# Optimization experiments

Measured on AMD Instinct MI355X. Metric: run time of the kernel, lower is better.

Reference implementation:

```python
import jax, jax.numpy as jnp
import numpy as np
import math

D_MODEL = 1024
N_HEADS = 16
D_HEAD = D_MODEL // N_HEADS
B, T = 2, 2048


def setup_inputs() -> dict:
    key = jax.random.key(0)
    ks = jax.random.split(key, 5)
    x = jax.random.normal(ks[0], (B, T, D_MODEL), dtype=jnp.float32)
    W_qkv = jax.random.normal(ks[1], (D_MODEL, 3 * D_MODEL), dtype=jnp.float32) * 0.02
    b_qkv = jnp.zeros((3 * D_MODEL,), dtype=jnp.float32)
    W_g = jax.random.normal(ks[2], (N_HEADS, D_HEAD, D_HEAD), dtype=jnp.float32) * 0.02
    W_out = jax.random.normal(ks[3], (D_MODEL, D_MODEL), dtype=jnp.float32) * 0.02
    b_out = jnp.zeros((D_MODEL,), dtype=jnp.float32)
    return {"x": x, "W_qkv": W_qkv, "b_qkv": b_qkv, "W_g": W_g, "W_out": W_out, "b_out": b_out}


def reference(x, W_qkv, b_qkv, W_g, W_out, b_out):
    b, t, d = x.shape
    h, dh = N_HEADS, D_HEAD
    qkv = x @ W_qkv + b_qkv                         # (B,T,3D)
    q, k, v = jnp.split(qkv, 3, axis=-1)
    # (B,T,D) -> (B,H,T,dh)
    q = q.reshape(b, t, h, dh).transpose(0, 2, 1, 3)
    k = k.reshape(b, t, h, dh).transpose(0, 2, 1, 3)
    v = v.reshape(b, t, h, dh).transpose(0, 2, 1, 3)
    scale = 1.0 / math.sqrt(dh)
    scores = jnp.einsum('bhtd,bhsd->bhts', q, k) * scale   # (B,H,T,T)
    causal = jnp.tril(jnp.ones((t, t), dtype=bool))
    scores = jnp.where(causal, scores, jnp.float32(-jnp.inf))
    attn = jax.nn.softmax(scores, axis=-1)
    # query-conditioned bilinear value gate (applied at each position)
    g = jax.nn.sigmoid(jnp.einsum('bhtd,hde->bhte', q, W_g))  # (B,H,T,dh)
    v = g * v
    out = jnp.einsum('bhts,bhsd->bhtd', attn, v)             # (B,H,T,dh)
    out = out.transpose(0, 2, 1, 3).reshape(b, t, d)
    return out @ W_out + b_out
```

## Files before the change

kernel.cpp:

```cpp
#include <hip/hip_runtime.h>
#include <hip/hip_bf16.h>

typedef unsigned short ushortT;
typedef __bf16 bf16x8 __attribute__((ext_vector_type(8)));
typedef __bf16 bf16x4 __attribute__((ext_vector_type(4)));
typedef float f32x4 __attribute__((ext_vector_type(4)));

#define T_SEQ 2048
#define DH 64
#define NH 16
#define DM 1024
#define TD 3072
#define BATCH 2
#define LOG2E 1.44269504f

__device__ inline ushortT f2bf(float f){
    union { float f; unsigned int u; } a; a.f = f;
    unsigned int r = a.u + 0x7fffu + ((a.u >> 16) & 1u);
    return (ushortT)(r >> 16);
}
__device__ inline float bf2f(ushortT u){
    union { float f; unsigned int u; } a; a.u = ((unsigned int)u) << 16;
    return a.f;
}

__device__ inline void gload_lds16(const void* g, void* l){
    __builtin_amdgcn_global_load_lds((const __attribute__((address_space(1))) void*)g,
                                     (__attribute__((address_space(3))) void*)l, 16, 0, 0);
}

__global__ __launch_bounds__(256) void cast_bf16_kernel(const float* __restrict__ in,
                                                        ushortT* __restrict__ out, int n){
    int i = (blockIdx.x * 256 + threadIdx.x) * 4;
    if (i < n){
        float4 v = *(const float4*)&in[i];
        out[i+0] = f2bf(v.x); out[i+1] = f2bf(v.y);
        out[i+2] = f2bf(v.z); out[i+3] = f2bf(v.w);
    }
}

__global__ __launch_bounds__(256) void transcast_kernel(const float* __restrict__ in,
                                                        ushortT* __restrict__ out, int K, int N){
    __shared__ float tile[64][65];
    int n0 = blockIdx.x * 64, k0 = blockIdx.y * 64;
    int tid = threadIdx.x;
    int c  = tid & 63;
    int r4 = tid >> 6;
#pragma unroll
    for (int i = 0; i < 16; i++){
        int k = r4 + i * 4;
        tile[k][c] = in[(size_t)(k0 + k) * N + n0 + c];
    }
    __syncthreads();
#pragma unroll
    for (int i = 0; i < 16; i++){
        int n = r4 + i * 4;
        out[(size_t)(n0 + n) * K + k0 + c] = f2bf(tile[c][n]);
    }
}

__global__ __launch_bounds__(256) void wg_transcast_kernel(const float* __restrict__ in,
                                                           ushortT* __restrict__ out){
    __shared__ float tile[64][65];
    int h = blockIdx.x;
    int tid = threadIdx.x;
    int c = tid & 63, r4 = tid >> 6;
#pragma unroll
    for (int i = 0; i < 16; i++){
        int d = r4 + i*4;
        tile[d][c] = in[h*4096 + d*64 + c];
    }
    __syncthreads();
#pragma unroll
    for (int i = 0; i < 16; i++){
        int e = r4 + i*4;
        out[h*4096 + e*64 + c] = f2bf(tile[c][e]);
    }
}

__device__ inline void store_out(ushortT* C, size_t i, float v){ C[i] = f2bf(v); }
__device__ inline void store_out(float*   C, size_t i, float v){ C[i] = v; }

template <typename OUT>
__global__ __launch_bounds__(256) void gemm_bf16_kernel(const ushortT* __restrict__ A,
                                                        const ushortT* __restrict__ BT,
                                                        const float* __restrict__ bias,
                                                        OUT* __restrict__ C,
                                                        int M, int N, int K){
    __shared__ __align__(16) ushortT As[2][128*32];
    __shared__ __align__(16) ushortT Bs[2][128*32];
    int tid = threadIdx.x;
    int m0 = blockIdx.x * 128;
    int n0 = blockIdx.y * 128;
    int wid = tid >> 6, lane = tid & 63;
    int l15 = lane & 15, g = lane >> 4;
    int wr = wid >> 1, wc = wid & 1;

    f32x4 acc[4][4];
#pragma unroll
    for (int i = 0; i < 4; i++)
#pragma unroll
        for (int j = 0; j < 4; j++) acc[i][j] = (f32x4){0.f,0.f,0.f,0.f};

    int srow = wid * 32 + (lane >> 2);
    int sch  = lane & 3;

#define GSTAGE(buf, k0)                                                                  \
    {                                                                                    \
        _Pragma("unroll")                                                                \
        for (int i_ = 0; i_ < 2; i_++){                                                  \
            int row_ = srow + i_ * 16;                                                   \
            const ushortT* asrc_ = A  + (size_t)(m0 + row_) * K + (k0) + sch * 8;        \
            const ushortT* bsrc_ = BT + (size_t)(n0 + row_) * K + (k0) + sch * 8;        \
            gload_lds16(asrc_, (char*)As[buf] + (wid*2 + i_) * 1024);                    \
            gload_lds16(bsrc_, (char*)Bs[buf] + (wid*2 + i_) * 1024);                    \
        }                                                                                \
    }

    GSTAGE(0, 0);
    __syncthreads();

    int nk = K >> 5;
    for (int kt = 0; kt < nk; kt++){
        int buf = kt & 1;
        if (kt + 1 < nk) GSTAGE(buf ^ 1, (kt + 1) * 32);

        bf16x8 af[4], bfr[4];
#pragma unroll
        for (int mi = 0; mi < 4; mi++){
            int r = wr*64 + mi*16 + l15;
            af[mi]  = *(const bf16x8*)(As[buf] + r*32 + g*8);
        }
#pragma unroll
        for (int ni = 0; ni < 4; ni++){
            int r = wc*64 + ni*16 + l15;
            bfr[ni] = *(const bf16x8*)(Bs[buf] + r*32 + g*8);
        }
#pragma unroll
        for (int mi = 0; mi < 4; mi++)
#pragma unroll
            for (int ni = 0; ni < 4; ni++)
                acc[mi][ni] = __builtin_amdgcn_mfma_f32_16x16x32_bf16(af[mi], bfr[ni], acc[mi][ni], 0, 0, 0);
        __syncthreads();
    }
#undef GSTAGE

#pragma unroll
    for (int mi = 0; mi < 4; mi++){
#pragma unroll
        for (int jj = 0; jj < 4; jj++){
            int mm = m0 + wr*64 + mi*16 + 4*g + jj;
#pragma unroll
            for (int ni = 0; ni < 4; ni++){
                int nn = n0 + wc*64 + ni*16 + l15;
                float v = acc[mi][ni][jj] + bias[nn];
                store_out(C, (size_t)mm * N + nn, v);
            }
        }
    }
}

__global__ __launch_bounds__(256) void gate_kernel(const ushortT* __restrict__ qkv,
                                                   const ushortT* __restrict__ WgT,
                                                   ushortT* __restrict__ vgT){
    __shared__ __align__(16) ushortT VT[64][72];
    int tblk = blockIdx.x, bh = blockIdx.y;
    int b = bh >> 4, h = bh & 15;
    int tid = threadIdx.x, wid = tid >> 6, lane = tid & 63;
    int l15 = lane & 15, g = lane >> 4;
    int t0 = tblk * 64;
    int tl = wid*16 + l15;

    const ushortT* qrow = qkv + ((size_t)b*T_SEQ + t0 + tl)*TD + h*DH;
    bf16x8 qf0 = *(const bf16x8*)(qrow + 8*g);
    bf16x8 qf1 = *(const bf16x8*)(qrow + 32 + 8*g);

    const ushortT* wbase = WgT + h*4096;
    const ushortT* vrow = qkv + ((size_t)b*T_SEQ + t0 + tl)*TD + 2*DM + h*DH;

#pragma unroll
    for (int ns = 0; ns < 4; ns++){
        int e = ns*16 + l15;
        bf16x8 wf0 = *(const bf16x8*)(wbase + e*64 + 8*g);
        bf16x8 wf1 = *(const bf16x8*)(wbase + e*64 + 32 + 8*g);
        f32x4 z = (f32x4){0.f,0.f,0.f,0.f};
        z = __builtin_amdgcn_mfma_f32_16x16x32_bf16(wf0, qf0, z, 0, 0, 0);
        z = __builtin_amdgcn_mfma_f32_16x16x32_bf16(wf1, qf1, z, 0, 0, 0);
        union { ushortT u[4]; uint2 v; } v4;
        v4.v = *(const uint2*)(vrow + ns*16 + 4*g);
#pragma unroll
        for (int jj = 0; jj < 4; jj++){
            float ex = __builtin_amdgcn_exp2f(-z[jj] * LOG2E);
            float gv = __builtin_amdgcn_rcpf(1.f + ex);
            VT[ns*16 + 4*g + jj][tl] = f2bf(gv * bf2f(v4.u[jj]));
        }
    }
    __syncthreads();
    for (int i = tid; i < 64*8; i += 256){
        int e = i >> 3, c8 = (i & 7) * 8;
        *(uint4*)&vgT[((size_t)bh * DH + e) * T_SEQ + t0 + c8] = *(const uint4*)&VT[e][c8];
    }
}

struct QState {
    bf16x8 qf0, qf1;
    float m_, lsum;
    f32x4 acc[4];
};

__device__ __forceinline__ void proc_tile(const ushortT* __restrict__ Kb,
                                          const ushortT* __restrict__ Vb,
                                          QState& S, bool diag,
                                          int wg, int l15, int g,
                                          ushortT (*Pl)[72], float* Al){
    f32x4 s[4];
    __builtin_amdgcn_s_setprio(1);
#pragma unroll
    for (int ns = 0; ns < 4; ns++){
        int kr = ns*16 + l15;
        bf16x8 kf0 = *(const bf16x8*)(Kb + kr*64 + ((g     ) ^ (kr & 7))*8);
        bf16x8 kf1 = *(const bf16x8*)(Kb + kr*64 + ((4 + g) ^ (kr & 7))*8);
        f32x4 z = (f32x4){0.f,0.f,0.f,0.f};
        z = __builtin_amdgcn_mfma_f32_16x16x32_bf16(kf0, S.qf0, z, 0, 0, 0);
        z = __builtin_amdgcn_mfma_f32_16x16x32_bf16(kf1, S.qf1, z, 0, 0, 0);
        s[ns] = z;
    }
    __builtin_amdgcn_s_setprio(0);

    float tmax = -INFINITY;
    if (diag){
        int qrel = wg*16 + l15;
#pragma unroll
        for (int ns = 0; ns < 4; ns++){
            int kbase = ns*16 + 4*g;
#pragma unroll
            for (int jj = 0; jj < 4; jj++){
                if (kbase + jj > qrel) s[ns][jj] = -INFINITY;
                tmax = fmaxf(tmax, s[ns][jj]);
            }
        }
    } else {
#pragma unroll
        for (int ns = 0; ns < 4; ns++){
            float a = fmaxf(s[ns][0], s[ns][1]);
            float c = fmaxf(s[ns][2], s[ns][3]);
            tmax = fmaxf(tmax, fmaxf(a, c));
        }
    }
    tmax = fmaxf(tmax, __shfl_xor(tmax, 16, 64));
    tmax = fmaxf(tmax, __shfl_xor(tmax, 32, 64));

    float mnew = fmaxf(S.m_, tmax);
    float mc = mnew * LOG2E;
    float rs = 0.f;
#pragma unroll
    for (int ns = 0; ns < 4; ns++){
        bf16x4 pk;
#pragma unroll
        for (int jj = 0; jj < 4; jj++){
            float p = __builtin_amdgcn_exp2f(fmaf(s[ns][jj], LOG2E, -mc));
            pk[jj] = (__bf16)p;
            rs += p;
        }
        *(bf16x4*)&Pl[l15][ns*16 + 4*g] = pk;
    }
    rs += __shfl_xor(rs, 16, 64);
    rs += __shfl_xor(rs, 32, 64);

    if (!__all(mnew == S.m_)){
        float alpha = __builtin_amdgcn_exp2f(fmaf(S.m_, LOG2E, -mc));
        Al[l15] = alpha;
        f32x4 a4 = *(const f32x4*)&Al[4*g];
#pragma unroll
        for (int nt = 0; nt < 4; nt++)
#pragma unroll
            for (int jj = 0; jj < 4; jj++) S.acc[nt][jj] *= a4[jj];
        S.lsum *= alpha;
        S.m_ = mnew;
    }
    S.lsum += rs;

    __builtin_amdgcn_s_setprio(1);
#pragma unroll
    for (int ks = 0; ks < 2; ks++){
        bf16x8 pa = *(const bf16x8*)&Pl[l15][ks*32 + 8*g];
#pragma unroll
        for (int nt = 0; nt < 4; nt++){
            int e = nt*16 + l15;
            bf16x8 vf = *(const bf16x8*)(Vb + e*64 + ((ks*4 + g) ^ (e & 7))*8);
            S.acc[nt] = __builtin_amdgcn_mfma_f32_16x16x32_bf16(pa, vf, S.acc[nt], 0, 0, 0);
        }
    }
    __builtin_amdgcn_s_setprio(0);
}

__global__ __launch_bounds__(512) void attn_kernel(const ushortT* __restrict__ qkv,
                                                   const ushortT* __restrict__ vgT,
                                                   ushortT* __restrict__ obf){
    __shared__ __align__(16) ushortT Ks[2][64*64];
    __shared__ __align__(16) ushortT Vs[2][64*64];
    __shared__ __align__(16) ushortT Plds[8][16][72];
    __shared__ __align__(16) float Alds[8][16];
    int bh = blockIdx.x, pairid = blockIdx.y;
    int b = bh >> 4, h = bh & 15;
    int tid = threadIdx.x, wid = tid >> 6, lane = tid & 63;
    int l15 = lane & 15, g = lane >> 4;
    int grp = wid >> 2, wg = wid & 3;

    const ushortT* Kg = qkv + (size_t)b * T_SEQ * TD + DM + h * DH;
    const ushortT* Vg = vgT + (size_t)bh * DH * T_SEQ;

    int st_row = wid*8 + (lane >> 3);
    int st_c   = (lane & 7) ^ ((lane >> 3) & 7);

#define STAGE_TILE(bufidx, kv0)                                                          \
    {                                                                                    \
        const ushortT* ksrc_ = Kg + (size_t)((kv0) + st_row) * TD + st_c*8;              \
        const ushortT* vsrc_ = Vg + (size_t)st_row * T_SEQ + (kv0) + st_c*8;             \
        gload_lds16(ksrc_, (char*)Ks[bufidx] + wid*1024);                                \
        gload_lds16(vsrc_, (char*)Vs[bufidx] + wid*1024);                                \
    }

    int pA = pairid, pB = 31 - pairid;
    int myp = grp ? pB : pA;

    QState S;
    {
        int qrow = myp*64 + wg*16 + l15;
        const ushortT* qb = qkv + ((size_t)b * T_SEQ + qrow) * TD + h * DH;
        S.qf0 = *(const bf16x8*)(qb + 8*g);
        S.qf1 = *(const bf16x8*)(qb + 32 + 8*g);
    }
#pragma unroll
    for (int j = 0; j < 8; j++){
        S.qf0[j] = (__bf16)((float)S.qf0[j] * 0.125f);
        S.qf1[j] = (__bf16)((float)S.qf1[j] * 0.125f);
    }
    S.m_ = -INFINITY; S.lsum = 0.f;
#pragma unroll
    for (int nt = 0; nt < 4; nt++) S.acc[nt] = (f32x4){0.f,0.f,0.f,0.f};

    STAGE_TILE(0, 0);
    __syncthreads();

    for (int t = 0; t <= pB; t++){
        int buf = t & 1;
        if (t < pB) STAGE_TILE(buf ^ 1, (t+1)*64);
        if (t <= myp)
            proc_tile(Ks[buf], Vs[buf], S, t == myp, wg, l15, g, Plds[wid], Alds[wid]);
        __syncthreads();
    }
#undef STAGE_TILE

    Alds[wid][l15] = 1.f / S.lsum;
    f32x4 i4 = *(const f32x4*)&Alds[wid][4*g];
#pragma unroll
    for (int jj = 0; jj < 4; jj++){
        int t = myp*64 + wg*16 + 4*g + jj;
#pragma unroll
        for (int nt = 0; nt < 4; nt++)
            obf[((size_t)b * T_SEQ + t) * DM + h*DH + nt*16 + l15] =
                f2bf(S.acc[nt][jj] * i4[jj]);
    }
}

extern "C" void kernel_launch(void* const* d_in, const int* in_sizes, int n_in,
                              void* d_out, int out_size, void* d_ws, size_t ws_size,
                              hipStream_t stream){
    const float* x    = (const float*)d_in[0];
    const float* Wqkv = (const float*)d_in[1];
    const float* bqkv = (const float*)d_in[2];
    const float* Wg   = (const float*)d_in[3];
    const float* Wout = (const float*)d_in[4];
    const float* bout = (const float*)d_in[5];

    char* ws = (char*)d_ws;
    ushortT* xbf   = (ushortT*)(ws);
    ushortT* wqkvT = (ushortT*)(ws + 8388608);
    ushortT* woutT = (ushortT*)(ws + 14680064);
    ushortT* qkvb  = (ushortT*)(ws + 16777216);
    ushortT* vgT   = (ushortT*)(ws + 41943040);
    ushortT* obf   = (ushortT*)(ws + 50331648);
    ushortT* wgT   = (ushortT*)(ws + 58720256);

    cast_bf16_kernel<<<4096, 256, 0, stream>>>(x, xbf, 4194304);
    transcast_kernel<<<dim3(48,16), 256, 0, stream>>>(Wqkv, wqkvT, 1024, 3072);
    transcast_kernel<<<dim3(16,16), 256, 0, stream>>>(Wout, woutT, 1024, 1024);
    wg_transcast_kernel<<<16, 256, 0, stream>>>(Wg, wgT);
    gemm_bf16_kernel<ushortT><<<dim3(32,24), 256, 0, stream>>>(xbf, wqkvT, bqkv, qkvb, 4096, 3072, 1024);
    gate_kernel<<<dim3(32,32), 256, 0, stream>>>(qkvb, wgT, vgT);
    attn_kernel<<<dim3(32,16), 512, 0, stream>>>(qkvb, vgT, obf);
    gemm_bf16_kernel<float><<<dim3(32,8), 256, 0, stream>>>(obf, woutT, bout, (float*)d_out, 4096, 1024, 1024);
}
```

Measured before the change: 126.4 us.

## Keep softmax probabilities in registers by permuting K rows and swapping MFMA operands

Staging now loads K rows in a permuted order, and the PV MFMA takes its operands swapped, so the exp'd score fragments already match the A-operand layout. The probabilities stay in registers instead of going through an LDS round trip, and the per-row alpha/inverse-sum broadcasts through LDS also go away. The output is written as packed 8-byte stores, and the grid is flattened to 1D with a remapped block-to-(bh,pair) order that may change scheduling balance and L2 locality. The permuted indexing and causal-mask offsets must agree exactly or the results will be wrong.

```diff
diff --git a/kernel.cpp b/kernel.cpp
--- a/kernel.cpp
+++ b/kernel.cpp
@@ -211,15 +211,15 @@
 __device__ __forceinline__ void proc_tile(const ushortT* __restrict__ Kb,
                                           const ushortT* __restrict__ Vb,
                                           QState& S, bool diag,
-                                          int wg, int l15, int g,
-                                          ushortT (*Pl)[72], float* Al){
+                                          int wg, int l15, int g){
+    int l7 = l15 & 7;
     f32x4 s[4];
     __builtin_amdgcn_s_setprio(1);
 #pragma unroll
     for (int ns = 0; ns < 4; ns++){
         int kr = ns*16 + l15;
-        bf16x8 kf0 = *(const bf16x8*)(Kb + kr*64 + ((g     ) ^ (kr & 7))*8);
-        bf16x8 kf1 = *(const bf16x8*)(Kb + kr*64 + ((4 + g) ^ (kr & 7))*8);
+        bf16x8 kf0 = *(const bf16x8*)(Kb + kr*64 + ((g    ) ^ l7)*8);
+        bf16x8 kf1 = *(const bf16x8*)(Kb + kr*64 + ((4 + g) ^ l7)*8);
         f32x4 z = (f32x4){0.f,0.f,0.f,0.f};
         z = __builtin_amdgcn_mfma_f32_16x16x32_bf16(kf0, S.qf0, z, 0, 0, 0);
         z = __builtin_amdgcn_mfma_f32_16x16x32_bf16(kf1, S.qf1, z, 0, 0, 0);
@@ -232,7 +232,7 @@
         int qrel = wg*16 + l15;
 #pragma unroll
         for (int ns = 0; ns < 4; ns++){
-            int kbase = ns*16 + 4*g;
+            int kbase = ((ns & 2) << 4) + 8*g + ((ns & 1) << 2);
 #pragma unroll
             for (int jj = 0; jj < 4; jj++){
                 if (kbase + jj > qrel) s[ns][jj] = -INFINITY;
@@ -253,28 +253,28 @@
     float mnew = fmaxf(S.m_, tmax);
     float mc = mnew * LOG2E;
     float rs = 0.f;
-#pragma unroll
-    for (int ns = 0; ns < 4; ns++){
-        bf16x4 pk;
-#pragma unroll
-        for (int jj = 0; jj < 4; jj++){
-            float p = __builtin_amdgcn_exp2f(fmaf(s[ns][jj], LOG2E, -mc));
-            pk[jj] = (__bf16)p;
-            rs += p;
-        }
-        *(bf16x4*)&Pl[l15][ns*16 + 4*g] = pk;
+    bf16x8 pa0, pa1;
+#pragma unroll
+    for (int jj = 0; jj < 4; jj++){
+        float p0 = __builtin_amdgcn_exp2f(fmaf(s[0][jj], LOG2E, -mc));
+        float p1 = __builtin_amdgcn_exp2f(fmaf(s[1][jj], LOG2E, -mc));
+        float p2 = __builtin_amdgcn_exp2f(fmaf(s[2][jj], LOG2E, -mc));
+        float p3 = __builtin_amdgcn_exp2f(fmaf(s[3][jj], LOG2E, -mc));
+        rs += (p0 + p1) + (p2 + p3);
+        pa0[jj]   = (__bf16)p0;
+        pa0[4+jj] = (__bf16)p1;
+        pa1[jj]   = (__bf16)p2;
+        pa1[4+jj] = (__bf16)p3;
     }
     rs += __shfl_xor(rs, 16, 64);
     rs += __shfl_xor(rs, 32, 64);
 
     if (!__all(mnew == S.m_)){
         float alpha = __builtin_amdgcn_exp2f(fmaf(S.m_, LOG2E, -mc));
-        Al[l15] = alpha;
-        f32x4 a4 = *(const f32x4*)&Al[4*g];
 #pragma unroll
         for (int nt = 0; nt < 4; nt++)
 #pragma unroll
-            for (int jj = 0; jj < 4; jj++) S.acc[nt][jj] *= a4[jj];
+            for (int jj = 0; jj < 4; jj++) S.acc[nt][jj] *= alpha;
         S.lsum *= alpha;
         S.m_ = mnew;
     }
@@ -283,12 +283,11 @@
     __builtin_amdgcn_s_setprio(1);
 #pragma unroll
     for (int ks = 0; ks < 2; ks++){
-        bf16x8 pa = *(const bf16x8*)&Pl[l15][ks*32 + 8*g];
+        bf16x8 pa = ks ? pa1 : pa0;
 #pragma unroll
         for (int nt = 0; nt < 4; nt++){
-            int e = nt*16 + l15;
-            bf16x8 vf = *(const bf16x8*)(Vb + e*64 + ((ks*4 + g) ^ (e & 7))*8);
-            S.acc[nt] = __builtin_amdgcn_mfma_f32_16x16x32_bf16(pa, vf, S.acc[nt], 0, 0, 0);
+            bf16x8 vf = *(const bf16x8*)(Vb + (nt*16 + l15)*64 + ((ks*4 + g) ^ l7)*8);
+            S.acc[nt] = __builtin_amdgcn_mfma_f32_16x16x32_bf16(vf, pa, S.acc[nt], 0, 0, 0);
         }
     }
     __builtin_amdgcn_s_setprio(0);
@@ -299,9 +298,11 @@
                                                    ushortT* __restrict__ obf){
     __shared__ __align__(16) ushortT Ks[2][64*64];
     __shared__ __align__(16) ushortT Vs[2][64*64];
-    __shared__ __align__(16) ushortT Plds[8][16][72];
-    __shared__ __align__(16) float Alds[8][16];
-    int bh = blockIdx.x, pairid = blockIdx.y;
+    int id = blockIdx.x;
+    int half = id >> 8, j = id & 255;
+    int bh = (half << 4) | (j >> 4);
+    int pp = j & 15;
+    int pairid = half ? (15 - pp) : pp;
     int b = bh >> 4, h = bh & 15;
     int tid = threadIdx.x, wid = tid >> 6, lane = tid & 63;
     int l15 = lane & 15, g = lane >> 4;
@@ -312,10 +313,11 @@
 
     int st_row = wid*8 + (lane >> 3);
     int st_c   = (lane & 7) ^ ((lane >> 3) & 7);
+    int st_prow = (st_row & 0x20) | ((st_row & 0x0C) << 1) | ((st_row & 0x10) >> 2) | (st_row & 3);
 
 #define STAGE_TILE(bufidx, kv0)                                                          \
     {                                                                                    \
-        const ushortT* ksrc_ = Kg + (size_t)((kv0) + st_row) * TD + st_c*8;              \
+        const ushortT* ksrc_ = Kg + (size_t)((kv0) + st_prow) * TD + st_c*8;             \
         const ushortT* vsrc_ = Vg + (size_t)st_row * T_SEQ + (kv0) + st_c*8;             \
         gload_lds16(ksrc_, (char*)Ks[bufidx] + wid*1024);                                \
         gload_lds16(vsrc_, (char*)Vs[bufidx] + wid*1024);                                \
@@ -332,9 +334,9 @@
         S.qf1 = *(const bf16x8*)(qb + 32 + 8*g);
     }
 #pragma unroll
-    for (int j = 0; j < 8; j++){
-        S.qf0[j] = (__bf16)((float)S.qf0[j] * 0.125f);
-        S.qf1[j] = (__bf16)((float)S.qf1[j] * 0.125f);
+    for (int jq = 0; jq < 8; jq++){
+        S.qf0[jq] = (__bf16)((float)S.qf0[jq] * 0.125f);
+        S.qf1[jq] = (__bf16)((float)S.qf1[jq] * 0.125f);
     }
     S.m_ = -INFINITY; S.lsum = 0.f;
 #pragma unroll
@@ -347,20 +349,19 @@
         int buf = t & 1;
         if (t < pB) STAGE_TILE(buf ^ 1, (t+1)*64);
         if (t <= myp)
-            proc_tile(Ks[buf], Vs[buf], S, t == myp, wg, l15, g, Plds[wid], Alds[wid]);
+            proc_tile(Ks[buf], Vs[buf], S, t == myp, wg, l15, g);
         __syncthreads();
     }
 #undef STAGE_TILE
 
-    Alds[wid][l15] = 1.f / S.lsum;
-    f32x4 i4 = *(const f32x4*)&Alds[wid][4*g];
-#pragma unroll
-    for (int jj = 0; jj < 4; jj++){
-        int t = myp*64 + wg*16 + 4*g + jj;
-#pragma unroll
-        for (int nt = 0; nt < 4; nt++)
-            obf[((size_t)b * T_SEQ + t) * DM + h*DH + nt*16 + l15] =
-                f2bf(S.acc[nt][jj] * i4[jj]);
+    float inv = 1.f / S.lsum;
+    size_t orow = ((size_t)b * T_SEQ + myp*64 + wg*16 + l15) * DM + h*DH;
+#pragma unroll
+    for (int nt = 0; nt < 4; nt++){
+        union { ushortT u[4]; uint2 v; } pk;
+#pragma unroll
+        for (int jj = 0; jj < 4; jj++) pk.u[jj] = f2bf(S.acc[nt][jj] * inv);
+        *(uint2*)&obf[orow + nt*16 + 4*g] = pk.v;
     }
 }
 
@@ -389,6 +390,6 @@
     wg_transcast_kernel<<<16, 256, 0, stream>>>(Wg, wgT);
     gemm_bf16_kernel<ushortT><<<dim3(32,24), 256, 0, stream>>>(xbf, wqkvT, bqkv, qkvb, 4096, 3072, 1024);
     gate_kernel<<<dim3(32,32), 256, 0, stream>>>(qkvb, wgT, vgT);
-    attn_kernel<<<dim3(32,16), 512, 0, stream>>>(qkvb, vgT, obf);
+    attn_kernel<<<512, 512, 0, stream>>>(qkvb, vgT, obf);
     gemm_bf16_kernel<float><<<dim3(32,8), 256, 0, stream>>>(obf, woutT, bout, (float*)d_out, 4096, 1024, 1024);
 }
```

Result: no change. 125.8 us (-0.4%).
